# Kernel optimization log

Measured on AMD Instinct MI355X. Metric: run time of the kernel, lower is better.

Reference implementation:

```python
import jax, jax.numpy as jnp
import numpy as np
from jax import lax

HEADS = 8
C, H, W = 64, 16, 16
D_K = C // HEADS
SCALE = 1.0 / np.sqrt(D_K * H * W).astype(np.float32)


def conv2d(x, w, b):
    # x: [N, C, H, W], w: [O, I, 3, 3], padding=1
    y = lax.conv_general_dilated(x, w, window_strides=(1, 1),
                                 padding=((1, 1), (1, 1)),
                                 dimension_numbers=('NCHW', 'OIHW', 'NCHW'))
    return y + b[None, :, None, None]


def _project(x, w, b, bs, seq):
    # x: [bs, seq, C, H, W] -> conv per frame -> [bs, heads, seq, d_k*H*W]
    y = conv2d(x.reshape(bs * seq, C, H, W), w, b)
    y = y.reshape(bs, seq, HEADS, D_K, H, W)
    y = jnp.transpose(y, (0, 2, 1, 3, 4, 5)).reshape(bs, HEADS, seq, D_K * H * W)
    return y


def setup_inputs() -> dict:
    key = jax.random.key(0)
    ks = jax.random.split(key, 11)
    shp = (2, 256, C, H, W)
    wstd = 1.0 / np.sqrt(C * 9)  # torch Conv2d default init scale
    inp = {
        'q': jax.random.normal(ks[0], shp, jnp.float32),
        'k': jax.random.normal(ks[1], shp, jnp.float32),
        'v': jax.random.normal(ks[2], shp, jnp.float32),
        'Wq': jax.random.uniform(ks[3], (C, C, 3, 3), jnp.float32, -wstd, wstd),
        'bq': jax.random.uniform(ks[4], (C,), jnp.float32, -wstd, wstd),
        'Wk': jax.random.uniform(ks[5], (C, C, 3, 3), jnp.float32, -wstd, wstd),
        'bk': jax.random.uniform(ks[6], (C,), jnp.float32, -wstd, wstd),
        'Wv': jax.random.uniform(ks[7], (C, C, 3, 3), jnp.float32, -wstd, wstd),
        'bv': jax.random.uniform(ks[8], (C,), jnp.float32, -wstd, wstd),
        'Wo': jax.random.uniform(ks[9], (C, C, 3, 3), jnp.float32, -wstd, wstd),
        'bo': jax.random.uniform(ks[10], (C,), jnp.float32, -wstd, wstd),
    }
    return inp


def reference(q, k, v, Wq, bq, Wk, bk, Wv, bv, Wo, bo):
    bs, seq = q.shape[0], q.shape[1]
    qh = _project(q, Wq, bq, bs, seq)  # [bs, h, seq, d_k*H*W]
    kh = _project(k, Wk, bk, bs, seq)
    vh = _project(v, Wv, bv, bs, seq)
    scores = jnp.einsum('bhqd,bhkd->bhqk', qh, kh) * SCALE
    attn = jax.nn.softmax(scores, axis=-1)
    out = jnp.einsum('bhqk,bhkd->bhqd', attn, vh)  # [bs, h, seq, d_k*H*W]
    out = out.reshape(bs, HEADS, seq, D_K, H, W)
    concat = jnp.transpose(out, (0, 2, 1, 3, 4, 5)).reshape(bs * seq, C, H, W)
    y = conv2d(concat, Wo, bo).reshape(bs, seq, C, H, W)
    return y
```

## Files before the change

### kernel.cpp

```cpp
#include <hip/hip_runtime.h>
#include <hip/hip_bf16.h>
#include <hip/hip_fp16.h>

typedef unsigned short u16;
typedef _Float16 f16x8 __attribute__((ext_vector_type(8)));
typedef u16 u16x8 __attribute__((ext_vector_type(8)));
typedef u16 u16x4 __attribute__((ext_vector_type(4)));
typedef float f32x4 __attribute__((ext_vector_type(4)));

__device__ __forceinline__ u16 f2h(float f){
  __half h = __float2half(f);
  return *(u16*)&h;
}

__device__ __forceinline__ void cp16_async(const u16* g, u16* l){
  __builtin_amdgcn_global_load_lds(
      (const __attribute__((address_space(1))) unsigned int*)g,
      (__attribute__((address_space(3))) unsigned int*)l,
      16, 0, 0);
}

__device__ __forceinline__ void prep_w_body(const float* W, u16* Wt, int i){
  if (i >= 36864) return;
  int co = i / 576, rem = i % 576, ci = rem / 9, tap = rem % 9;
  int n = co >> 4, lr = co & 15, kk = ci >> 5, lg = (ci >> 3) & 3, j = ci & 7;
  int s = tap*2 + kk;
  Wt[(((s*4 + n)*64) + lg*16 + lr)*8 + j] = f2h(W[i]);
}

__global__ __launch_bounds__(256) void prep_w3(
    const float* __restrict__ Wq, const float* __restrict__ Wk,
    const float* __restrict__ Wv, u16* __restrict__ Wt)
{
  int which = blockIdx.y;
  const float* W = (which == 0) ? Wq : (which == 1) ? Wk : Wv;
  prep_w_body(W, Wt + which*36864, blockIdx.x * 256 + threadIdx.x);
}

__global__ __launch_bounds__(256) void prep_w(
    const float* __restrict__ W, u16* __restrict__ Wt)
{
  prep_w_body(W, Wt, blockIdx.x * 256 + threadIdx.x);
}

template<bool IN_F32, bool OUT_PROJ>
__device__ __forceinline__ void conv_body(
    const void* __restrict__ xin, const u16* __restrict__ Wt,
    const float* __restrict__ bias, void* __restrict__ dst,
    int frame, u16* xT, float* stage, int tid)
{
  #define STAGE_Q(qi, buf) do {                                             \
    if (IN_F32){                                                            \
      const float* src_ = (const float*)xin + (size_t)frame*16384 + (qi)*4096; \
      _Pragma("unroll")                                                     \
      for (int t_ = 0; t_ < 4; ++t_){                                       \
        int c_ = tid + t_*256;                                              \
        cp16_async((const u16*)(src_ + c_*4), (u16*)((float*)(buf) + c_*4));\
      }                                                                     \
    } else {                                                                \
      const u16* src_ = (const u16*)xin + (size_t)frame*16384 + (qi)*4096;  \
      _Pragma("unroll")                                                     \
      for (int t_ = 0; t_ < 2; ++t_){                                       \
        int c_ = tid + t_*256;                                              \
        cp16_async(src_ + c_*8, (u16*)(buf) + c_*8);                        \
      }                                                                     \
    }                                                                       \
  } while(0)

  float* S0 = stage;
  float* S1 = stage + 4096;

  STAGE_Q(0, S0);
  for (int i = tid; i < 2592; i += 256)
    *(uint4*)((char*)xT + i*16) = make_uint4(0u, 0u, 0u, 0u);
  __syncthreads();

  const int p = tid, py = p >> 4, px = p & 15;
  const int pp = (py + 1)*18 + px + 1;

  #pragma unroll 1
  for (int qi = 0; qi < 4; ++qi){
    if (qi < 3) STAGE_Q(qi + 1, (qi & 1) ? S0 : S1);
    const float* Sf = (qi & 1) ? S1 : S0;
    const u16*   Su = (const u16*)Sf;
    #pragma unroll
    for (int b = 0; b < 2; ++b){
      u16x8 pk;
      #pragma unroll
      for (int j = 0; j < 8; ++j)
        pk[j] = IN_F32 ? f2h(Sf[(b*8 + j)*256 + p]) : Su[(b*8 + j)*256 + p];
      unsigned cb = (unsigned)(qi*2 + b);
      unsigned off = (unsigned)(pp*128) + (((cb + (unsigned)pp) & 7u) << 4);
      *(u16x8*)((char*)xT + off) = pk;
    }
    __syncthreads();
  }

  const int w = tid >> 6, lane = tid & 63, lr = lane & 15, lg = lane >> 4;
  const int pyb = w * 4;

  f32x4 acc[4][4];
  #pragma unroll
  for (int n = 0; n < 4; ++n){
    float b = bias[n*16 + lr];
    #pragma unroll
    for (int m = 0; m < 4; ++m){
      acc[m][n][0] = b; acc[m][n][1] = b; acc[m][n][2] = b; acc[m][n][3] = b;
    }
  }

  #define LOADB(s, B) do {                                                  \
    _Pragma("unroll")                                                       \
    for (int n_ = 0; n_ < 4; ++n_)                                          \
      B[n_] = *(const f16x8*)(Wt + ((((s)*4 + n_)*64) + lane)*8);           \
  } while(0)

  #define STEP(s, B) do {                                                   \
    int tap_ = (s) >> 1, kk_ = (s) & 1;                                     \
    int dy_ = tap_ / 3, dx_ = tap_ - dy_*3;                                 \
    f16x8 af_[4];                                                           \
    _Pragma("unroll")                                                       \
    for (int m_ = 0; m_ < 4; ++m_){                                         \
      int pp_ = (pyb + m_ + dy_)*18 + lr + dx_;                             \
      unsigned slot_ = ((unsigned)(kk_*4 + lg) + (unsigned)pp_) & 7u;       \
      af_[m_] = *(const f16x8*)((const char*)xT                             \
                 + (unsigned)(pp_*128) + (slot_ << 4));                     \
    }                                                                       \
    _Pragma("unroll")                                                       \
    for (int m_ = 0; m_ < 4; ++m_)                                          \
      _Pragma("unroll")                                                     \
      for (int n_ = 0; n_ < 4; ++n_)                                        \
        acc[m_][n_] = __builtin_amdgcn_mfma_f32_16x16x32_f16(               \
            af_[m_], B[n_], acc[m_][n_], 0, 0, 0);                          \
  } while(0)

  f16x8 Ba[4], Bb[4];
  LOADB(0, Ba);
  #pragma unroll 1
  for (int it = 0; it < 9; ++it){
    LOADB(it*2 + 1, Bb);
    STEP(it*2, Ba);
    if (it < 8) LOADB(it*2 + 2, Ba);
    STEP(it*2 + 1, Bb);
  }
  #undef LOADB
  #undef STEP
  #undef STAGE_Q

  if (OUT_PROJ){
    u16* d = (u16*)dst;
    const int b = frame >> 8, sq = frame & 255;
    #pragma unroll
    for (int n = 0; n < 4; ++n){
      int co = n*16 + lr, h = co >> 3, dk = co & 7;
      size_t base = ((size_t)((b*8 + h)*256 + sq))*2048 + dk*256;
      #pragma unroll
      for (int m = 0; m < 4; ++m){
        int P = w*64 + m*16 + lg*4;
        u16x4 o4;
        #pragma unroll
        for (int r = 0; r < 4; ++r) o4[r] = f2h(acc[m][n][r]);
        *(u16x4*)(d + base + P) = o4;
      }
    }
  } else {
    float* d = (float*)dst + (size_t)frame * 16384;
    #pragma unroll
    for (int n = 0; n < 4; ++n){
      int co = n*16 + lr;
      #pragma unroll
      for (int m = 0; m < 4; ++m){
        int P = w*64 + m*16 + lg*4;
        *(f32x4*)(d + co*256 + P) = acc[m][n];
      }
    }
  }
}

__global__ __launch_bounds__(256, 2) void conv3_mfma(
    const float* __restrict__ q, const float* __restrict__ k,
    const float* __restrict__ v, const u16* __restrict__ Wt3,
    const float* __restrict__ bq, const float* __restrict__ bk,
    const float* __restrict__ bv,
    u16* __restrict__ qh, u16* __restrict__ kh, u16* __restrict__ vh)
{
  __shared__ __align__(16) u16 xT[324 * 64];
  __shared__ __align__(16) float stage[2*4096];
  const int which = blockIdx.x >> 9;
  const int frame = blockIdx.x & 511;
  const float* x = (which == 0) ? q : (which == 1) ? k : v;
  const float* bias = (which == 0) ? bq : (which == 1) ? bk : bv;
  u16* dst = (which == 0) ? qh : (which == 1) ? kh : vh;
  conv_body<true, true>(x, Wt3 + which*36864, bias, dst, frame, xT, stage, threadIdx.x);
}

__global__ __launch_bounds__(256, 2) void conv_out_mfma(
    const u16* __restrict__ xin, const u16* __restrict__ Wt,
    const float* __restrict__ bias, float* __restrict__ out)
{
  __shared__ __align__(16) u16 xT[324 * 64];
  __shared__ __align__(16) float stage[2*4096];
  conv_body<false, false>(xin, Wt, bias, out, blockIdx.x, xT, stage, threadIdx.x);
}

__global__ __launch_bounds__(256) void transpose_v(
    const u16* __restrict__ vh, u16* __restrict__ vt)
{
  __shared__ u16 tile[64][72];
  const int tid = threadIdx.x;
  const int dt = blockIdx.x, st = blockIdx.y, bh = blockIdx.z;
  {
    int r = tid >> 2, c4 = tid & 3;
    const u16* src = vh + ((size_t)(bh*256 + st*64 + r))*2048 + dt*64 + c4*16;
    uint4 v0 = *(const uint4*)src;
    uint4 v1 = *(const uint4*)(src + 8);
    *(uint4*)&tile[r][c4*16]     = v0;
    *(uint4*)&tile[r][c4*16 + 8] = v1;
  }
  __syncthreads();
  {
    int dr = tid >> 2, s4 = tid & 3;
    u16 tmp[16];
    #pragma unroll
    for (int i = 0; i < 16; ++i) tmp[i] = tile[s4*16 + i][dr];
    u16* dstp = vt + ((size_t)(bh*2048 + dt*64 + dr))*256 + st*64 + s4*16;
    *(uint4*)dstp       = *(uint4*)&tmp[0];
    *(uint4*)(dstp + 8) = *(uint4*)&tmp[8];
  }
}

__global__ __launch_bounds__(512, 2) void attn_kernel(
    const u16* __restrict__ qh, const u16* __restrict__ kh,
    const u16* __restrict__ vt, u16* __restrict__ obuf)
{
  const float SCALE = 0.022097086912079608f;
  __shared__ __align__(16) u16 Qs[16*2048];
  __shared__ __align__(16) u16 Kb[2][16384];
  __shared__ __align__(16) u16 P[16*256];
  __shared__ float redA[8][16];
  __shared__ float redB[8][16];

  const int tid = threadIdx.x;
  const int w = tid >> 6, lane = tid & 63, lr = lane & 15, lg = lane >> 4;

  const int id = blockIdx.x;
  const int xcd = id & 7, j = id >> 3;
  const int bh = xcd + 8*(j & 1), qt = j >> 1;
  const int q0 = qt * 16, b = bh >> 3, h = bh & 7;

  const u16* Qg = qh + ((size_t)(bh*256 + q0))*2048;
  const u16* Kg = kh + (size_t)bh * 256 * 2048;
  const u16* Vg = vt + (size_t)bh * 2048 * 256;

  const int spK = (lane & 7) ^ ((lane >> 3) & 7);
  #define STAGE_K(c, buf)                                                   \
    _Pragma("unroll")                                                       \
    for (int r_ = 0; r_ < 4; ++r_)                                          \
      cp16_async(Kg + (size_t)(w*32 + r_*8 + (lane>>3))*2048 + (c)*64 + spK*8, \
                 (buf) + w*2048 + r_*512);

  #define STAGE_V(c, buf)                                                   \
    _Pragma("unroll")                                                       \
    for (int r_ = 0; r_ < 8; ++r_){                                         \
      int rl_ = w*16 + r_*2 + (lane>>5);                                    \
      int sp_ = (lane & 31) ^ (rl_ & 7);                                    \
      cp16_async(Vg + (size_t)((c)*128 + rl_)*256 + sp_*8,                  \
                 (buf) + w*4096 + r_*512);                                  \
    }

  #pragma unroll
  for (int r = 0; r < 8; ++r){
    int t = r*64 + lane;
    int row = w*2 + (t >> 8);
    int dp = t & 255;
    int sp = (dp & ~7) | ((dp & 7) ^ (row & 7));
    cp16_async(Qg + (size_t)row*2048 + sp*8, Qs + w*4096 + r*512);
  }
  STAGE_K(0, Kb[0]);
  __syncthreads();

  const f32x4 zero4 = {0.f, 0.f, 0.f, 0.f};
  f32x4 sacc[2] = {zero4, zero4};
  #pragma unroll 1
  for (int c = 0; c < 32; ++c){
    if (c < 31) STAGE_K(c+1, Kb[(c+1)&1]);
    const u16* kb = Kb[c&1];
    #pragma unroll
    for (int d2 = 0; d2 < 2; ++d2){
      unsigned aoff = (((unsigned)lr << 12) + (unsigned)(c*128 + d2*64 + lg*16))
                      ^ (unsigned)((lr & 7) << 4);
      f16x8 a = *(const f16x8*)((const char*)Qs + aoff);
      #pragma unroll
      for (int n = 0; n < 2; ++n){
        int row = w*32 + n*16 + lr;
        const u16* kp = kb + row*64 + (((d2*4 + lg) ^ (row & 7)) << 3);
        f16x8 bk = *(const f16x8*)kp;
        sacc[n] = __builtin_amdgcn_mfma_f32_16x16x32_f16(a, bk, sacc[n], 0,0,0);
      }
    }
    __syncthreads();
  }

  float mx[4];
  #pragma unroll
  for (int r = 0; r < 4; ++r){
    float vv = fmaxf(sacc[0][r], sacc[1][r]);
    #pragma unroll
    for (int off = 1; off < 16; off <<= 1) vv = fmaxf(vv, __shfl_xor(vv, off));
    mx[r] = vv;
  }
  if (lr == 0){
    #pragma unroll
    for (int r = 0; r < 4; ++r) redA[w][lg*4 + r] = mx[r];
  }
  __syncthreads();
  #pragma unroll
  for (int r = 0; r < 4; ++r){
    int row = lg*4 + r;
    float vv = redA[0][row];
    #pragma unroll
    for (int ww = 1; ww < 8; ++ww) vv = fmaxf(vv, redA[ww][row]);
    mx[r] = vv;
  }

  const int kbase = w * 32;
  float sm[4] = {0.f, 0.f, 0.f, 0.f};
  #pragma unroll
  for (int n = 0; n < 2; ++n)
    #pragma unroll
    for (int r = 0; r < 4; ++r){
      float pv = __expf((sacc[n][r] - mx[r]) * SCALE);
      sm[r] += pv;
      int row = lg*4 + r;
      int col = kbase + n*16 + lr;
      unsigned off = (((unsigned)row << 9) + ((unsigned)col << 1))
                     ^ (unsigned)((row & 7) << 4);
      *(u16*)((char*)P + off) = f2h(pv);
    }
  #pragma unroll
  for (int r = 0; r < 4; ++r){
    float vv = sm[r];
    #pragma unroll
    for (int off = 1; off < 16; off <<= 1) vv += __shfl_xor(vv, off);
    sm[r] = vv;
  }
  if (lr == 0){
    #pragma unroll
    for (int r = 0; r < 4; ++r) redB[w][lg*4 + r] = sm[r];
  }
  __syncthreads();
  float rs[4];
  #pragma unroll
  for (int r = 0; r < 4; ++r){
    int row = lg*4 + r;
    float s = redB[0][row];
    #pragma unroll
    for (int ww = 1; ww < 8; ++ww) s += redB[ww][row];
    rs[r] = 1.0f / s;
  }

  u16* Vb0 = Qs;
  u16* Vb1 = &Kb[0][0];
  STAGE_V(0, Vb0);
  __syncthreads();
  #pragma unroll 1
  for (int c = 0; c < 16; ++c){
    if (c < 15){
      u16* nbuf = ((c+1) & 1) ? Vb1 : Vb0;
      STAGE_V(c+1, nbuf);
    }
    const u16* vb = (c & 1) ? Vb1 : Vb0;
    f32x4 oacc = zero4;
    #pragma unroll
    for (int kt = 0; kt < 8; ++kt){
      unsigned poff = (((unsigned)lr << 9) + (unsigned)(kt*64 + lg*16))
                      ^ (unsigned)((lr & 7) << 4);
      f16x8 pa = *(const f16x8*)((const char*)P + poff);
      int row = w*16 + lr;
      const u16* vp = vb + row*256 + (((kt*4 + lg) ^ (row & 7)) << 3);
      f16x8 bv = *(const f16x8*)vp;
      oacc = __builtin_amdgcn_mfma_f32_16x16x32_f16(pa, bv, oacc, 0,0,0);
    }
    #pragma unroll
    for (int r = 0; r < 4; ++r){
      float o = oacc[r] * rs[r];
      int qrow = q0 + lg*4 + r;
      int d = c*128 + w*16 + lr;
      int frame = b*256 + qrow;
      int cdim = h*8 + (d >> 8);
      obuf[((size_t)(frame*64 + cdim))*256 + (d & 255)] = f2h(o);
    }
    __syncthreads();
  }
  #undef STAGE_K
  #undef STAGE_V
}

extern "C" void kernel_launch(void* const* d_in, const int* in_sizes, int n_in,
                              void* d_out, int out_size, void* d_ws, size_t ws_size,
                              hipStream_t stream)
{
  const float* q  = (const float*)d_in[0];
  const float* k  = (const float*)d_in[1];
  const float* v  = (const float*)d_in[2];
  const float* Wq = (const float*)d_in[3];
  const float* bq = (const float*)d_in[4];
  const float* Wk = (const float*)d_in[5];
  const float* bk = (const float*)d_in[6];
  const float* Wv = (const float*)d_in[7];
  const float* bv = (const float*)d_in[8];
  const float* Wo = (const float*)d_in[9];
  const float* bo = (const float*)d_in[10];
  float* out = (float*)d_out;

  char* ws = (char*)d_ws;
  u16* qh = (u16*)(ws);
  u16* kh = (u16*)(ws + (size_t)16*1024*1024);
  u16* vh = (u16*)(ws + (size_t)32*1024*1024);
  u16* vt = (u16*)(ws + (size_t)48*1024*1024);
  u16* obuf = vh;
  u16* Wt3  = vt;
  u16* WtO  = qh;

  prep_w3<<<dim3(144, 3), dim3(256), 0, stream>>>(Wq, Wk, Wv, Wt3);
  conv3_mfma<<<dim3(1536), dim3(256), 0, stream>>>(q, k, v, Wt3, bq, bk, bv,
                                                   qh, kh, vh);
  transpose_v<<<dim3(32, 4, 16), dim3(256), 0, stream>>>(vh, vt);
  attn_kernel<<<dim3(256), dim3(512), 0, stream>>>(qh, kh, vt, obuf);
  prep_w<<<dim3(144), dim3(256), 0, stream>>>(Wo, WtO);
  conv_out_mfma<<<dim3(512), dim3(256), 0, stream>>>(obuf, WtO, bo, out);
}
```

Before: 127.0 us.

## Use 512-thread conv blocks and overlap second channel-half staging with MFMA

The conv kernels now run with 512 threads (8 waves), each wave computing 2 output rows instead of 4, which halves the per-wave accumulators and allows higher occupancy. Input staging is split into two channel halves. The second half's async global load is issued while the MFMA K-loop runs over the first half, replacing the old four-quarter staging loop that synchronised after every quarter. The K-loop is fully unrolled over taps. The risks are more waves competing for LDS, and each wave re-loading the full weight fragments for only half the work.

```diff
diff --git a/kernel.cpp b/kernel.cpp
--- a/kernel.cpp
+++ b/kernel.cpp
@@ -49,62 +49,55 @@
     const float* __restrict__ bias, void* __restrict__ dst,
     int frame, u16* xT, float* stage, int tid)
 {
-  #define STAGE_Q(qi, buf) do {                                             \
+  #define STAGE_H(h) do {                                                   \
     if (IN_F32){                                                            \
-      const float* src_ = (const float*)xin + (size_t)frame*16384 + (qi)*4096; \
+      const float* src_ = (const float*)xin + (size_t)frame*16384 + (h)*8192; \
       _Pragma("unroll")                                                     \
       for (int t_ = 0; t_ < 4; ++t_){                                       \
-        int c_ = tid + t_*256;                                              \
-        cp16_async((const u16*)(src_ + c_*4), (u16*)((float*)(buf) + c_*4));\
+        int c_ = tid + t_*512;                                              \
+        cp16_async((const u16*)(src_ + c_*4), (u16*)(stage + c_*4));        \
       }                                                                     \
     } else {                                                                \
-      const u16* src_ = (const u16*)xin + (size_t)frame*16384 + (qi)*4096;  \
+      const u16* src_ = (const u16*)xin + (size_t)frame*16384 + (h)*8192;   \
       _Pragma("unroll")                                                     \
       for (int t_ = 0; t_ < 2; ++t_){                                       \
-        int c_ = tid + t_*256;                                              \
-        cp16_async(src_ + c_*8, (u16*)(buf) + c_*8);                        \
+        int c_ = tid + t_*512;                                              \
+        cp16_async(src_ + c_*8, (u16*)stage + c_*8);                        \
       }                                                                     \
     }                                                                       \
   } while(0)
 
-  float* S0 = stage;
-  float* S1 = stage + 4096;
-
-  STAGE_Q(0, S0);
-  for (int i = tid; i < 2592; i += 256)
-    *(uint4*)((char*)xT + i*16) = make_uint4(0u, 0u, 0u, 0u);
-  __syncthreads();
-
-  const int p = tid, py = p >> 4, px = p & 15;
+  const int p = tid & 255, ph = tid >> 8;
+  const int py = p >> 4, px = p & 15;
   const int pp = (py + 1)*18 + px + 1;
 
-  #pragma unroll 1
-  for (int qi = 0; qi < 4; ++qi){
-    if (qi < 3) STAGE_Q(qi + 1, (qi & 1) ? S0 : S1);
-    const float* Sf = (qi & 1) ? S1 : S0;
-    const u16*   Su = (const u16*)Sf;
-    #pragma unroll
-    for (int b = 0; b < 2; ++b){
-      u16x8 pk;
-      #pragma unroll
-      for (int j = 0; j < 8; ++j)
-        pk[j] = IN_F32 ? f2h(Sf[(b*8 + j)*256 + p]) : Su[(b*8 + j)*256 + p];
-      unsigned cb = (unsigned)(qi*2 + b);
-      unsigned off = (unsigned)(pp*128) + (((cb + (unsigned)pp) & 7u) << 4);
-      *(u16x8*)((char*)xT + off) = pk;
-    }
-    __syncthreads();
-  }
+  #define TRANSP(h) do {                                                    \
+    const float* Sf_ = stage;                                               \
+    const u16*   Su_ = (const u16*)stage;                                   \
+    _Pragma("unroll")                                                       \
+    for (int t_ = 0; t_ < 2; ++t_){                                         \
+      int cbl_ = ph*2 + t_;                                                 \
+      u16x8 pk_;                                                            \
+      _Pragma("unroll")                                                     \
+      for (int j_ = 0; j_ < 8; ++j_){                                       \
+        int cl_ = cbl_*8 + j_;                                              \
+        pk_[j_] = IN_F32 ? f2h(Sf_[cl_*256 + p]) : Su_[cl_*256 + p];        \
+      }                                                                     \
+      unsigned cb_ = (unsigned)((h)*4 + cbl_);                              \
+      unsigned off_ = (unsigned)(pp*128) + (((cb_ + (unsigned)pp) & 7u) << 4); \
+      *(u16x8*)((char*)xT + off_) = pk_;                                    \
+    }                                                                       \
+  } while(0)
 
   const int w = tid >> 6, lane = tid & 63, lr = lane & 15, lg = lane >> 4;
-  const int pyb = w * 4;
-
-  f32x4 acc[4][4];
+  const int pyb = w * 2;
+
+  f32x4 acc[2][4];
   #pragma unroll
   for (int n = 0; n < 4; ++n){
     float b = bias[n*16 + lr];
     #pragma unroll
-    for (int m = 0; m < 4; ++m){
+    for (int m = 0; m < 2; ++m){
       acc[m][n][0] = b; acc[m][n][1] = b; acc[m][n][2] = b; acc[m][n][3] = b;
     }
   }
@@ -118,34 +111,59 @@
   #define STEP(s, B) do {                                                   \
     int tap_ = (s) >> 1, kk_ = (s) & 1;                                     \
     int dy_ = tap_ / 3, dx_ = tap_ - dy_*3;                                 \
-    f16x8 af_[4];                                                           \
-    _Pragma("unroll")                                                       \
-    for (int m_ = 0; m_ < 4; ++m_){                                         \
+    f16x8 af_[2];                                                           \
+    _Pragma("unroll")                                                       \
+    for (int m_ = 0; m_ < 2; ++m_){                                         \
       int pp_ = (pyb + m_ + dy_)*18 + lr + dx_;                             \
       unsigned slot_ = ((unsigned)(kk_*4 + lg) + (unsigned)pp_) & 7u;       \
       af_[m_] = *(const f16x8*)((const char*)xT                             \
                  + (unsigned)(pp_*128) + (slot_ << 4));                     \
     }                                                                       \
     _Pragma("unroll")                                                       \
-    for (int m_ = 0; m_ < 4; ++m_)                                          \
+    for (int m_ = 0; m_ < 2; ++m_)                                          \
       _Pragma("unroll")                                                     \
       for (int n_ = 0; n_ < 4; ++n_)                                        \
         acc[m_][n_] = __builtin_amdgcn_mfma_f32_16x16x32_f16(               \
             af_[m_], B[n_], acc[m_][n_], 0, 0, 0);                          \
   } while(0)
 
-  f16x8 Ba[4], Bb[4];
-  LOADB(0, Ba);
-  #pragma unroll 1
-  for (int it = 0; it < 9; ++it){
-    LOADB(it*2 + 1, Bb);
-    STEP(it*2, Ba);
-    if (it < 8) LOADB(it*2 + 2, Ba);
-    STEP(it*2 + 1, Bb);
-  }
+  #define KLOOP(kk) do {                                                    \
+    f16x8 Ba[4], Bb[4];                                                     \
+    LOADB((kk), Ba);                                                        \
+    _Pragma("unroll")                                                       \
+    for (int tap = 0; tap < 9; ++tap){                                      \
+      if (tap & 1){                                                         \
+        if (tap + 1 < 9) LOADB(((tap+1)*2 + (kk)), Ba);                     \
+        STEP((tap*2 + (kk)), Bb);                                           \
+      } else {                                                              \
+        if (tap + 1 < 9) LOADB(((tap+1)*2 + (kk)), Bb);                     \
+        STEP((tap*2 + (kk)), Ba);                                           \
+      }                                                                     \
+    }                                                                       \
+  } while(0)
+
+  STAGE_H(0);
+  for (int i = tid; i < 2592; i += 512)
+    *(uint4*)((char*)xT + i*16) = make_uint4(0u, 0u, 0u, 0u);
+  __syncthreads();
+
+  TRANSP(0);
+  __syncthreads();
+
+  STAGE_H(1);
+  KLOOP(0);
+  __syncthreads();
+
+  TRANSP(1);
+  __syncthreads();
+
+  KLOOP(1);
+
+  #undef STAGE_H
+  #undef TRANSP
   #undef LOADB
   #undef STEP
-  #undef STAGE_Q
+  #undef KLOOP
 
   if (OUT_PROJ){
     u16* d = (u16*)dst;
@@ -155,8 +173,8 @@
       int co = n*16 + lr, h = co >> 3, dk = co & 7;
       size_t base = ((size_t)((b*8 + h)*256 + sq))*2048 + dk*256;
       #pragma unroll
-      for (int m = 0; m < 4; ++m){
-        int P = w*64 + m*16 + lg*4;
+      for (int m = 0; m < 2; ++m){
+        int P = w*32 + m*16 + lg*4;
         u16x4 o4;
         #pragma unroll
         for (int r = 0; r < 4; ++r) o4[r] = f2h(acc[m][n][r]);
@@ -169,15 +187,15 @@
     for (int n = 0; n < 4; ++n){
       int co = n*16 + lr;
       #pragma unroll
-      for (int m = 0; m < 4; ++m){
-        int P = w*64 + m*16 + lg*4;
+      for (int m = 0; m < 2; ++m){
+        int P = w*32 + m*16 + lg*4;
         *(f32x4*)(d + co*256 + P) = acc[m][n];
       }
     }
   }
 }
 
-__global__ __launch_bounds__(256, 2) void conv3_mfma(
+__global__ __launch_bounds__(512, 4) void conv3_mfma(
     const float* __restrict__ q, const float* __restrict__ k,
     const float* __restrict__ v, const u16* __restrict__ Wt3,
     const float* __restrict__ bq, const float* __restrict__ bk,
@@ -185,7 +203,7 @@
     u16* __restrict__ qh, u16* __restrict__ kh, u16* __restrict__ vh)
 {
   __shared__ __align__(16) u16 xT[324 * 64];
-  __shared__ __align__(16) float stage[2*4096];
+  __shared__ __align__(16) float stage[8192];
   const int which = blockIdx.x >> 9;
   const int frame = blockIdx.x & 511;
   const float* x = (which == 0) ? q : (which == 1) ? k : v;
@@ -194,12 +212,12 @@
   conv_body<true, true>(x, Wt3 + which*36864, bias, dst, frame, xT, stage, threadIdx.x);
 }
 
-__global__ __launch_bounds__(256, 2) void conv_out_mfma(
+__global__ __launch_bounds__(512, 4) void conv_out_mfma(
     const u16* __restrict__ xin, const u16* __restrict__ Wt,
     const float* __restrict__ bias, float* __restrict__ out)
 {
   __shared__ __align__(16) u16 xT[324 * 64];
-  __shared__ __align__(16) float stage[2*4096];
+  __shared__ __align__(16) float stage[8192];
   conv_body<false, false>(xin, Wt, bias, out, blockIdx.x, xT, stage, threadIdx.x);
 }
 
@@ -423,10 +441,10 @@
   u16* WtO  = qh;
 
   prep_w3<<<dim3(144, 3), dim3(256), 0, stream>>>(Wq, Wk, Wv, Wt3);
-  conv3_mfma<<<dim3(1536), dim3(256), 0, stream>>>(q, k, v, Wt3, bq, bk, bv,
+  conv3_mfma<<<dim3(1536), dim3(512), 0, stream>>>(q, k, v, Wt3, bq, bk, bv,
                                                    qh, kh, vh);
   transpose_v<<<dim3(32, 4, 16), dim3(256), 0, stream>>>(vh, vt);
   attn_kernel<<<dim3(256), dim3(512), 0, stream>>>(qh, kh, vt, obuf);
   prep_w<<<dim3(144), dim3(256), 0, stream>>>(Wo, WtO);
-  conv_out_mfma<<<dim3(512), dim3(256), 0, stream>>>(obuf, WtO, bo, out);
-}
+  conv_out_mfma<<<dim3(512), dim3(512), 0, stream>>>(obuf, WtO, bo, out);
+}
```

Result: slower. 130.5 us (+2.8%).
